# Performance work log

Measured on AMD Instinct MI355X. Metric: run time of the kernel, lower is better.

Reference implementation:

```python
import jax, jax.numpy as jnp
import numpy as np
import math

HIDDEN = 1024
N_HEAD = 16
D_K = HIDDEN // N_HEAD

def setup_inputs() -> dict:
    key = jax.random.key(0)
    ks = jax.random.split(key, 6)
    B, T = 2, 2048
    x = jax.random.normal(ks[0], (B, T, HIDDEN), dtype=jnp.float32)
    mask = jax.random.randint(ks[1], (B, 1, 1, T), 0, 2, dtype=jnp.int32)
    s = 1.0 / math.sqrt(HIDDEN)
    W_qkv = jax.random.normal(ks[2], (HIDDEN, 3 * HIDDEN), dtype=jnp.float32) * s
    b_qkv = jnp.zeros((3 * HIDDEN,), dtype=jnp.float32)
    W_out = jax.random.normal(ks[3], (HIDDEN, HIDDEN), dtype=jnp.float32) * s
    b_out = jnp.zeros((HIDDEN,), dtype=jnp.float32)
    return {"x": x, "mask": mask, "W_qkv": W_qkv, "b_qkv": b_qkv, "W_out": W_out, "b_out": b_out}

def reference(x, mask, W_qkv, b_qkv, W_out, b_out):
    B, T, H = x.shape
    qkv = x @ W_qkv + b_qkv  # [B,T,3H]
    q, k, v = jnp.split(qkv, 3, axis=-1)
    # [B,T,H] -> [B,nh,T,dk]
    def split_heads(t):
        return t.reshape(B, T, N_HEAD, D_K).transpose(0, 2, 1, 3)
    q, k, v = split_heads(q), split_heads(k), split_heads(v)
    scores = jnp.einsum('bhqd,bhkd->bhqk', q, k) / math.sqrt(D_K)
    scores = jnp.where(mask == 0, jnp.float32(-1e9), scores)
    attn = jax.nn.softmax(scores, axis=-1)
    out = jnp.einsum('bhqk,bhkd->bhqd', attn, v)
    out = out.transpose(0, 2, 1, 3).reshape(B, T, H)
    return out @ W_out + b_out
```

## Files before the change

### kernel.cpp

```cpp
#include <hip/hip_runtime.h>
#include <stdint.h>

typedef unsigned short u16;
typedef unsigned int u32;
typedef short bf16x8 __attribute__((ext_vector_type(8)));
typedef float f32x4 __attribute__((ext_vector_type(4)));

#define MFMA16(a, b, c) __builtin_amdgcn_mfma_f32_16x16x32_bf16((a), (b), (c), 0, 0, 0)
#define BAR()                              \
  do {                                     \
    __builtin_amdgcn_sched_barrier(0);     \
    __builtin_amdgcn_s_barrier();          \
    __builtin_amdgcn_sched_barrier(0);     \
  } while (0)

__device__ __forceinline__ u16 f2bf(float f) {
  union { float f; u32 u; } v; v.f = f;
  u32 u = v.u;
  u32 r = (u + 0x7FFFu + ((u >> 16) & 1u)) >> 16;
  return (u16)r;
}
__device__ __forceinline__ float bf2f(u16 h) {
  union { u32 u; float f; } v; v.u = ((u32)h) << 16;
  return v.f;
}
__device__ __forceinline__ u32 cvtpk_bf16(float lo, float hi) {
  u32 r;
  asm("v_cvt_pk_bf16_f32 %0, %1, %2" : "=v"(r) : "v"(lo), "v"(hi));
  return r;
}

__device__ __forceinline__ void gload_lds16(const void* g, void* l) {
  __builtin_amdgcn_global_load_lds(
      (const __attribute__((address_space(1))) unsigned int*)g,
      (__attribute__((address_space(3))) unsigned int*)l,
      16, 0, 0);
}

__global__ __launch_bounds__(256) void transpose_f32_bf16(
    const float* __restrict__ src, u16* __restrict__ dst, int R, int C) {
  __shared__ u16 t[32][33];
  const int bx = blockIdx.x * 32, by = blockIdx.y * 32;
  const int tx = threadIdx.x & 31, ty = threadIdx.x >> 5;
#pragma unroll
  for (int i = 0; i < 32; i += 8)
    t[ty + i][tx] = f2bf(src[(size_t)(by + ty + i) * C + bx + tx]);
  __syncthreads();
#pragma unroll
  for (int i = 0; i < 32; i += 8)
    dst[(size_t)(bx + ty + i) * R + by + tx] = t[tx][ty + i];
}

__global__ __launch_bounds__(512) void mask_compact(
    const int* __restrict__ mask, int* __restrict__ idx, int* __restrict__ cnt) {
  const int b = blockIdx.x;
  const int tid = threadIdx.x;
  const int lane = tid & 63, wave = tid >> 6;
  __shared__ int wtot[8];
  int m[4], c = 0;
#pragma unroll
  for (int j = 0; j < 4; ++j) {
    m[j] = (mask[b * 2048 + tid * 4 + j] != 0);
    c += m[j];
  }
  int pfx = c;
#pragma unroll
  for (int sh = 1; sh < 64; sh <<= 1) {
    int v = __shfl_up(pfx, sh);
    if (lane >= sh) pfx += v;
  }
  if (lane == 63) wtot[wave] = pfx;
  int epfx = pfx - c;
  __syncthreads();
  int wbase = 0, total = 0;
#pragma unroll
  for (int w = 0; w < 8; ++w) {
    int v = wtot[w];
    if (w < wave) wbase += v;
    total += v;
  }
  int pos = b * 2048 + wbase + epfx;
#pragma unroll
  for (int j = 0; j < 4; ++j)
    if (m[j]) idx[pos++] = tid * 4 + j;
  for (int i = total + tid; i < 2048; i += 512) idx[b * 2048 + i] = 0;
  if (tid == 0) cnt[b] = total;
}

__global__ __launch_bounds__(256) void gemm_a32_bf16(
    const float* __restrict__ A, const u16* __restrict__ Bt,
    const float* __restrict__ bias, u16* __restrict__ Cout,
    int M, int N, int K) {
  __shared__ __align__(16) u16 As[2][128 * 64];
  __shared__ __align__(16) u16 Bs[2][128 * 64];
  const int tid = threadIdx.x;
  const int lane = tid & 63;
  const int wave = tid >> 6;
  const int nwg = gridDim.x;
  const int id = blockIdx.x;
  const int sw = (id & 7) * (nwg >> 3) + (id >> 3);
  const int nx = N >> 7;
  const int m0 = (sw / nx) * 128;
  const int n0 = (sw % nx) * 128;
  const int wm = (wave >> 1) * 64;
  const int wn = (wave & 1) * 64;

  f32x4 acc[4][4] = {};
  const char* Bbase = (const char*)Bt;
  float4 fa[4], fb[4];

#define A32_ISSUE_B(ktile, buf)                                                \
  _Pragma("unroll") for (int i = 0; i < 4; ++i) {                              \
    int flat = wave * 1024 + lane * 16 + i * 4096;                             \
    int row = flat >> 7;                                                       \
    int cb = flat & 127;                                                       \
    int scb = cb ^ ((row & 7) << 4);                                           \
    gload_lds16(Bbase + ((size_t)(n0 + row) * K + (ktile)) * 2 + scb,          \
                (char*)&Bs[buf][0] + flat);                                    \
  }

#define A32_LOAD_A(ktile)                                                      \
  _Pragma("unroll") for (int i = 0; i < 4; ++i) {                              \
    int flat = wave * 1024 + lane * 16 + i * 4096;                             \
    int row = flat >> 7;                                                       \
    int cb = flat & 127;                                                       \
    const float* ax = A + (size_t)(m0 + row) * K + (ktile) + (cb >> 1);        \
    fa[i] = *(const float4*)ax;                                                \
    fb[i] = *(const float4*)(ax + 4);                                          \
  }

#define A32_CVT(buf)                                                           \
  _Pragma("unroll") for (int i = 0; i < 4; ++i) {                              \
    int flat = wave * 1024 + lane * 16 + i * 4096;                             \
    int row = flat >> 7;                                                       \
    int cb = flat & 127;                                                       \
    union { u32 w[4]; bf16x8 v; } o;                                           \
    o.w[0] = cvtpk_bf16(fa[i].x, fa[i].y);                                     \
    o.w[1] = cvtpk_bf16(fa[i].z, fa[i].w);                                     \
    o.w[2] = cvtpk_bf16(fb[i].x, fb[i].y);                                     \
    o.w[3] = cvtpk_bf16(fb[i].z, fb[i].w);                                     \
    *(bf16x8*)((char*)&As[buf][0] + row * 128 + (cb ^ ((row & 7) << 4))) = o.v; \
  }

  A32_ISSUE_B(0, 0);
  A32_LOAD_A(0);
  A32_CVT(0);
  asm volatile("s_waitcnt lgkmcnt(0)" ::: "memory");
  BAR();

  const int nsteps = K >> 6;
  for (int t = 0; t < nsteps; ++t) {
    if (t < nsteps - 1) {
      A32_ISSUE_B((t << 6) + 64, (t & 1) ^ 1);
      A32_LOAD_A((t << 6) + 64);
    }
    __builtin_amdgcn_sched_barrier(0);
#pragma unroll
    for (int ks = 0; ks < 2; ++ks) {
      const int col = (lane >> 4) * 8 + ks * 32;
      bf16x8 af[4], bfr[4];
#pragma unroll
      for (int mt = 0; mt < 4; ++mt) {
        int row = wm + mt * 16 + (lane & 15);
        af[mt] = *(const bf16x8*)((const char*)&As[t & 1][0] + row * 128 +
                                  ((col * 2) ^ ((row & 7) << 4)));
      }
#pragma unroll
      for (int nt = 0; nt < 4; ++nt) {
        int row = wn + nt * 16 + (lane & 15);
        bfr[nt] = *(const bf16x8*)((const char*)&Bs[t & 1][0] + row * 128 +
                                   ((col * 2) ^ ((row & 7) << 4)));
      }
#pragma unroll
      for (int mt = 0; mt < 4; ++mt)
#pragma unroll
        for (int nt = 0; nt < 4; ++nt)
          acc[mt][nt] = MFMA16(af[mt], bfr[nt], acc[mt][nt]);
    }
    __builtin_amdgcn_sched_barrier(0);
    if (t < nsteps - 1) {
      A32_CVT((t & 1) ^ 1);
      asm volatile("s_waitcnt lgkmcnt(0)" ::: "memory");
      BAR();
    }
  }
#undef A32_ISSUE_B
#undef A32_LOAD_A
#undef A32_CVT

  float bv[4];
#pragma unroll
  for (int nt = 0; nt < 4; ++nt)
    bv[nt] = bias[n0 + wn + nt * 16 + (lane & 15)];
#pragma unroll
  for (int mt = 0; mt < 4; ++mt)
#pragma unroll
    for (int nt = 0; nt < 4; ++nt)
#pragma unroll
      for (int r = 0; r < 4; ++r) {
        int m = m0 + wm + mt * 16 + (lane >> 4) * 4 + r;
        int n = n0 + wn + nt * 16 + (lane & 15);
        Cout[(size_t)m * N + n] = f2bf(acc[mt][nt][r] + bv[nt]);
      }
}

template <bool OUT_BF16>
__global__ __launch_bounds__(256) void gemm_bf16(
    const u16* __restrict__ A, const u16* __restrict__ Bt,
    const float* __restrict__ bias, void* __restrict__ Cout,
    int M, int N, int K) {
  __shared__ __align__(16) u16 As[2][128 * 64];
  __shared__ __align__(16) u16 Bs[2][128 * 64];
  const int tid = threadIdx.x;
  const int lane = tid & 63;
  const int wave = tid >> 6;
  const int nwg = gridDim.x;
  const int id = blockIdx.x;
  const int sw = (id & 7) * (nwg >> 3) + (id >> 3);
  const int nx = N >> 7;
  const int m0 = (sw / nx) * 128;
  const int n0 = (sw % nx) * 128;
  const int wm = (wave >> 1) * 64;
  const int wn = (wave & 1) * 64;

  f32x4 acc[4][4] = {};

  const char* Abase = (const char*)A;
  const char* Bbase = (const char*)Bt;

#define STAGE_AB(ktile, buf)                                                   \
  _Pragma("unroll") for (int i = 0; i < 4; ++i) {                              \
    int flat = wave * 1024 + lane * 16 + i * 4096;                             \
    int row = flat >> 7;                                                       \
    int cb = flat & 127;                                                       \
    int scb = cb ^ ((row & 7) << 4);                                           \
    gload_lds16(Abase + ((size_t)(m0 + row) * K + (ktile)) * 2 + scb,          \
                (char*)&As[buf][0] + flat);                                    \
    gload_lds16(Bbase + ((size_t)(n0 + row) * K + (ktile)) * 2 + scb,          \
                (char*)&Bs[buf][0] + flat);                                    \
  }

  STAGE_AB(0, 0);

  const int nsteps = K >> 6;
  for (int t = 0; t < nsteps; ++t) {
    asm volatile("s_waitcnt vmcnt(0)" ::: "memory");
    BAR();
    if (t < nsteps - 1) STAGE_AB((t << 6) + 64, (t & 1) ^ 1);
#pragma unroll
    for (int ks = 0; ks < 2; ++ks) {
      const int col = (lane >> 4) * 8 + ks * 32;
      bf16x8 af[4], bfr[4];
#pragma unroll
      for (int mt = 0; mt < 4; ++mt) {
        int row = wm + mt * 16 + (lane & 15);
        af[mt] = *(const bf16x8*)((const char*)&As[t & 1][0] + row * 128 +
                                  ((col * 2) ^ ((row & 7) << 4)));
      }
#pragma unroll
      for (int nt = 0; nt < 4; ++nt) {
        int row = wn + nt * 16 + (lane & 15);
        bfr[nt] = *(const bf16x8*)((const char*)&Bs[t & 1][0] + row * 128 +
                                   ((col * 2) ^ ((row & 7) << 4)));
      }
#pragma unroll
      for (int mt = 0; mt < 4; ++mt)
#pragma unroll
        for (int nt = 0; nt < 4; ++nt)
          acc[mt][nt] = MFMA16(af[mt], bfr[nt], acc[mt][nt]);
    }
  }
#undef STAGE_AB

  float bv[4];
#pragma unroll
  for (int nt = 0; nt < 4; ++nt)
    bv[nt] = bias[n0 + wn + nt * 16 + (lane & 15)];
#pragma unroll
  for (int mt = 0; mt < 4; ++mt)
#pragma unroll
    for (int nt = 0; nt < 4; ++nt)
#pragma unroll
      for (int r = 0; r < 4; ++r) {
        int m = m0 + wm + mt * 16 + (lane >> 4) * 4 + r;
        int n = n0 + wn + nt * 16 + (lane & 15);
        float v = acc[mt][nt][r] + bv[nt];
        if (OUT_BF16)
          ((u16*)Cout)[(size_t)m * N + n] = f2bf(v);
        else
          ((float*)Cout)[(size_t)m * N + n] = v;
      }
}

#define T_SEQ 2048
#define ROWQKV 3072
#define SCL 0.180336880f

template <bool SPLIT>
__global__ __launch_bounds__(512) void attn_fwd(
    const u16* __restrict__ qkv, const int* __restrict__ idx,
    const int* __restrict__ cnt, u16* __restrict__ outp,
    float* __restrict__ Ml) {
  __shared__ __align__(16) u16 Ks[2][2][64 * 64];
  __shared__ __align__(16) u16 Vt[2][2][64 * 64];
  __shared__ __align__(16) u32 lut[256 * 4];

  const int tid = threadIdx.x;
  const int lane = tid & 63;
  const int wave = tid >> 6;
  const int r15 = lane & 15;
  const int g = lane >> 4;
  const int id = blockIdx.x;
  const int hz = ((id >> 6) << 3) | (id & 7);
  const int qb = (id >> 3) & 7;
  const int h = SPLIT ? (hz >> 2) : (hz >> 1);
  const int z = SPLIT ? (hz & 3) : (hz & 1);
  const int split = SPLIT ? (z >> 1) : 0;
  const int b = SPLIT ? (z & 1) : z;
  const int q0 = qb * 256 + wave * 32;
  const size_t rowb = (size_t)b * T_SEQ;
  const int* idxb = idx + b * 2048;
  const int count = cnt[b];
  const int ntot = (count + 127) >> 7;
  const int nth = (ntot + 1) >> 1;
  const int t0 = (SPLIT && split) ? nth : 0;
  const int nt2 = SPLIT ? (split ? ntot - nth : nth) : ntot;

  for (int i = tid; i < 256; i += 512) {
    union { u32 w[4]; bf16x8 v; } e;
#pragma unroll
    for (int j = 0; j < 4; ++j)
      e.w[j] = (((i >> (2 * j)) & 1) ? 0x3F80u : 0u) |
               (((i >> (2 * j + 1)) & 1) ? 0x3F800000u : 0u);
    *(bf16x8*)((char*)lut + i * 16) = e.v;
  }

  bf16x8 aq[2][2];
#pragma unroll
  for (int mt = 0; mt < 2; ++mt)
#pragma unroll
    for (int ks = 0; ks < 2; ++ks) {
      bf16x8 t = *(const bf16x8*)(qkv +
          (rowb + q0 + mt * 16 + r15) * ROWQKV + h * 64 + g * 8 + ks * 32);
#pragma unroll
      for (int j = 0; j < 8; ++j) t[j] = (short)f2bf(bf2f((u16)t[j]) * SCL);
      aq[mt][ks] = t;
    }

  f32x4 accO[2][4] = {};
  f32x4 ssum[2] = {};
  bf16x8 vr0, vr1;

#define ISSUE_K2(ct, buf)                                                      \
  {                                                                            \
    int L = wave * 1024 + lane * 16;                                           \
    int row = L >> 7;                                                          \
    int cb = L & 127;                                                          \
    int scb = cb ^ ((row & 7) << 4);                                           \
    int prow = ((row >> 4) & 1) * 32 + ((row >> 2) & 3) * 8 +                  \
               (row >> 5) * 4 + (row & 3);                                     \
    int gk0 = idxb[(ct) * 128 + prow];                                         \
    int gk1 = idxb[(ct) * 128 + 64 + prow];                                    \
    gload_lds16((const char*)qkv +                                             \
                    ((rowb + gk0) * ROWQKV + 1024 + h * 64) * 2 + scb,         \
                (char*)&Ks[buf][0][0] + wave * 1024);                          \
    gload_lds16((const char*)qkv +                                             \
                    ((rowb + gk1) * ROWQKV + 1024 + h * 64) * 2 + scb,         \
                (char*)&Ks[buf][1][0] + wave * 1024);                          \
  }

#define LOAD_V2(ct)                                                            \
  {                                                                            \
    int key = tid >> 3;                                                        \
    int gv0 = idxb[(ct) * 128 + key];                                          \
    int gv1 = idxb[(ct) * 128 + 64 + key];                                     \
    vr0 = *(const bf16x8*)(qkv + (rowb + gv0) * ROWQKV + 2048 + h * 64 +       \
                           (tid & 7) * 8);                                     \
    vr1 = *(const bf16x8*)(qkv + (rowb + gv1) * ROWQKV + 2048 + h * 64 +       \
                           (tid & 7) * 8);                                     \
  }

#define WRITE_V2(buf, ct)                                                      \
  {                                                                            \
    int key = tid >> 3;                                                        \
    if ((ct) * 128 + key >= count) {                                           \
      bf16x8 zz = {};                                                          \
      vr0 = zz;                                                                \
    }                                                                          \
    if ((ct) * 128 + 64 + key >= count) {                                      \
      bf16x8 zz = {};                                                          \
      vr1 = zz;                                                                \
    }                                                                          \
    _Pragma("unroll") for (int j = 0; j < 8; ++j) {                            \
      int row = (tid & 7) * 8 + j;                                             \
      int sv = ((row ^ (row >> 3)) & 7) << 4;                                  \
      *(u16*)((char*)&Vt[buf][0][0] + row * 128 + ((key * 2) ^ sv)) =          \
          (u16)vr0[j];                                                         \
      *(u16*)((char*)&Vt[buf][1][0] + row * 128 + ((key * 2) ^ sv)) =          \
          (u16)vr1[j];                                                         \
    }                                                                          \
  }

#define COMPUTE_HALF(H, ct)                                                    \
  {                                                                            \
    f32x4 s[2][4] = {};                                                        \
    _Pragma("unroll") for (int ks = 0; ks < 2; ++ks) {                         \
      bf16x8 bk[4];                                                            \
      _Pragma("unroll") for (int nt = 0; nt < 4; ++nt) {                       \
        int row = nt * 16 + r15;                                               \
        int cb = (g * 8 + ks * 32) * 2;                                        \
        bk[nt] = *(const bf16x8*)((const char*)&Ks[cur][H][0] + row * 128 +    \
                                  (cb ^ ((row & 7) << 4)));                    \
      }                                                                        \
      _Pragma("unroll") for (int mt = 0; mt < 2; ++mt)                         \
        _Pragma("unroll") for (int nt = 0; nt < 4; ++nt)                       \
          s[mt][nt] = MFMA16(bk[nt], aq[mt][ks], s[mt][nt]);                   \
    }                                                                          \
    u32 pk[2][4][2];                                                           \
    _Pragma("unroll") for (int mt = 0; mt < 2; ++mt)                           \
      _Pragma("unroll") for (int nt = 0; nt < 4; ++nt) {                       \
        float e0 = exp2f(s[mt][nt][0]);                                        \
        float e1 = exp2f(s[mt][nt][1]);                                        \
        float e2 = exp2f(s[mt][nt][2]);                                        \
        float e3 = exp2f(s[mt][nt][3]);                                        \
        pk[mt][nt][0] = cvtpk_bf16(e0, e1);                                    \
        pk[mt][nt][1] = cvtpk_bf16(e2, e3);                                    \
      }                                                                        \
    __builtin_amdgcn_s_setprio(1);                                             \
    _Pragma("unroll") for (int ks = 0; ks < 2; ++ks) {                         \
      const int col = g * 8 + ks * 32;                                         \
      bf16x8 bv[4];                                                            \
      _Pragma("unroll") for (int nt = 0; nt < 4; ++nt) {                       \
        int row = nt * 16 + r15;                                               \
        int sv = ((row ^ (row >> 3)) & 7) << 4;                                \
        bv[nt] = *(const bf16x8*)((const char*)&Vt[cur][H][0] + row * 128 +    \
                                  ((col * 2) ^ sv));                           \
      }                                                                        \
      int rbase = count - ((ct) * 128 + (H) * 64 + ks * 32 + g * 8);           \
      int rr = rbase < 0 ? 0 : (rbase > 8 ? 8 : rbase);                        \
      u32 lb = (1u << rr) - 1u;                                                \
      bf16x8 mf = *(const bf16x8*)((const char*)lut + lb * 16);                \
      _Pragma("unroll") for (int mt = 0; mt < 2; ++mt) {                       \
        union { u32 w[4]; bf16x8 v; } ap;                                      \
        ap.w[0] = pk[mt][ks][0];                                               \
        ap.w[1] = pk[mt][ks][1];                                               \
        ap.w[2] = pk[mt][2 + ks][0];                                           \
        ap.w[3] = pk[mt][2 + ks][1];                                           \
        _Pragma("unroll") for (int nt = 0; nt < 4; ++nt)                       \
          accO[mt][nt] = MFMA16(ap.v, bv[nt], accO[mt][nt]);                   \
        ssum[mt] = MFMA16(ap.v, mf, ssum[mt]);                                 \
      }                                                                        \
    }                                                                          \
    __builtin_amdgcn_s_setprio(0);                                             \
  }

  if (nt2 > 0) {
    ISSUE_K2(t0, 0);
    LOAD_V2(t0);
    __syncthreads();
    WRITE_V2(0, t0);
    asm volatile("s_waitcnt lgkmcnt(0)" ::: "memory");
    BAR();

    int cur = 0;
    for (int t = 0; t < nt2; ++t) {
      const int ct = t0 + t;
      if (t < nt2 - 1) {
        ISSUE_K2(ct + 1, cur ^ 1);
        LOAD_V2(ct + 1);
      }

      COMPUTE_HALF(0, ct);
      COMPUTE_HALF(1, ct);

      if (t < nt2 - 1) {
        asm volatile("s_waitcnt vmcnt(0)" ::: "memory");
        WRITE_V2(cur ^ 1, ct + 1);
        asm volatile("s_waitcnt lgkmcnt(0)" ::: "memory");
        BAR();
        cur ^= 1;
      }
    }
  }

  if (SPLIT) {
    u16* po = outp + (size_t)split * T_SEQ * 2 * 1024;
#pragma unroll
    for (int mt = 0; mt < 2; ++mt) {
#pragma unroll
      for (int r = 0; r < 4; ++r) {
        int q = q0 + mt * 16 + g * 4 + r;
#pragma unroll
        for (int nt = 0; nt < 4; ++nt)
          po[(rowb + q) * 1024 + h * 64 + nt * 16 + r15] = f2bf(accO[mt][nt][r]);
      }
      if (r15 == 0) {
        int idxm = ((split * 2 + b) * 16 + h) * T_SEQ + q0 + mt * 16 + g * 4;
        *(f32x4*)(Ml + idxm) = ssum[mt];
      }
    }
  } else {
#pragma unroll
    for (int mt = 0; mt < 2; ++mt)
#pragma unroll
      for (int r = 0; r < 4; ++r) {
        float inv = 1.f / ssum[mt][r];
        int q = q0 + mt * 16 + g * 4 + r;
#pragma unroll
        for (int nt = 0; nt < 4; ++nt)
          outp[(rowb + q) * 1024 + h * 64 + nt * 16 + r15] =
              f2bf(accO[mt][nt][r] * inv);
      }
  }
#undef ISSUE_K2
#undef LOAD_V2
#undef WRITE_V2
#undef COMPUTE_HALF
}

__global__ __launch_bounds__(256) void attn_combine(
    const u16* __restrict__ part, const float* __restrict__ Ml,
    u16* __restrict__ att) {
  int idx = blockIdx.x * 256 + threadIdx.x;
  int row = idx >> 7;
  int c8 = idx & 127;
  int col = c8 * 8;
  int h = c8 >> 3;
  int b = row >> 11, q = row & 2047;
  float l0 = Ml[(b * 16 + h) * T_SEQ + q];
  float l1 = Ml[((2 + b) * 16 + h) * T_SEQ + q];
  float inv = 1.f / (l0 + l1);
  bf16x8 o0 = *(const bf16x8*)(part + (size_t)row * 1024 + col);
  bf16x8 o1 = *(const bf16x8*)(part + (size_t)T_SEQ * 2 * 1024 +
                               (size_t)row * 1024 + col);
  bf16x8 o;
#pragma unroll
  for (int j = 0; j < 8; ++j)
    o[j] = (short)f2bf((bf2f((u16)o0[j]) + bf2f((u16)o1[j])) * inv);
  *(bf16x8*)(att + (size_t)row * 1024 + col) = o;
}

extern "C" void kernel_launch(void* const* d_in, const int* in_sizes, int n_in,
                              void* d_out, int out_size, void* d_ws, size_t ws_size,
                              hipStream_t stream) {
  const float* x = (const float*)d_in[0];
  const int* mask = (const int*)d_in[1];
  const float* Wqkv = (const float*)d_in[2];
  const float* bqkv = (const float*)d_in[3];
  const float* Wout = (const float*)d_in[4];
  const float* bout = (const float*)d_in[5];
  float* out = (float*)d_out;

  const int B = 2, T = 2048, H = 1024, M = B * T;

  u16* qkv = (u16*)d_ws;
  u16* att = qkv + (size_t)M * 3 * H;
  u16* WtQ = att + (size_t)M * H;
  u16* WtO = WtQ + (size_t)3 * H * H;
  u16* part = WtO + (size_t)H * H;
  float* Ml = (float*)(part + (size_t)2 * M * H);
  int* idxb = (int*)(Ml + (size_t)2 * 131072);
  int* cntb = idxb + B * T;

  const size_t need = ((size_t)M * 3 * H + (size_t)M * H + (size_t)3 * H * H +
                       (size_t)H * H + (size_t)2 * M * H) * 2 +
                      (size_t)2 * 131072 * 4 + (size_t)(B * T + 8) * 4;
  const bool split = ws_size >= need;

  transpose_f32_bf16<<<dim3(3 * H / 32, H / 32), 256, 0, stream>>>(Wqkv, WtQ, H, 3 * H);
  transpose_f32_bf16<<<dim3(H / 32, H / 32), 256, 0, stream>>>(Wout, WtO, H, H);
  mask_compact<<<B, 512, 0, stream>>>(mask, idxb, cntb);
  gemm_a32_bf16<<<(3 * H / 128) * (M / 128), 256, 0, stream>>>(x, WtQ, bqkv, qkv, M, 3 * H, H);
  if (split) {
    attn_fwd<true><<<512, 512, 0, stream>>>(qkv, idxb, cntb, part, Ml);
    attn_combine<<<(M * H / 8 + 255) / 256, 256, 0, stream>>>(part, Ml, att);
  } else {
    attn_fwd<false><<<256, 512, 0, stream>>>(qkv, idxb, cntb, att, Ml);
  }
  gemm_bf16<false><<<(H / 128) * (M / 128), 256, 0, stream>>>(att, WtO, bout, out, M, H, H);
}
```

Baseline: 133.5 us.

## Deepen QKV GEMM prefetch to two k-tiles ahead with triple-buffered B

Adds a third LDS buffer for B and a second set of fp32 A staging registers so global loads run two k-steps ahead of compute instead of one. The loop is unrolled by two to alternate the register sets. This is meant to hide more global-memory latency behind the MFMA work. The cost is extra LDS and more registers, which may lower occupancy. The loop also assumes nsteps is even.

```diff
diff --git a/kernel.cpp b/kernel.cpp
--- a/kernel.cpp
+++ b/kernel.cpp
@@ -92,7 +92,7 @@
     const float* __restrict__ bias, u16* __restrict__ Cout,
     int M, int N, int K) {
   __shared__ __align__(16) u16 As[2][128 * 64];
-  __shared__ __align__(16) u16 Bs[2][128 * 64];
+  __shared__ __align__(16) u16 Bs[3][128 * 64];
   const int tid = threadIdx.x;
   const int lane = tid & 63;
   const int wave = tid >> 6;
@@ -107,7 +107,7 @@
 
   f32x4 acc[4][4] = {};
   const char* Bbase = (const char*)Bt;
-  float4 fa[4], fb[4];
+  float4 fa0[4], fb0[4], fa1[4], fb1[4];
 
 #define A32_ISSUE_B(ktile, buf)                                                \
   _Pragma("unroll") for (int i = 0; i < 4; ++i) {                              \
@@ -119,71 +119,80 @@
                 (char*)&Bs[buf][0] + flat);                                    \
   }
 
-#define A32_LOAD_A(ktile)                                                      \
+#define A32_LOAD_A(ktile, FA, FB)                                              \
   _Pragma("unroll") for (int i = 0; i < 4; ++i) {                              \
     int flat = wave * 1024 + lane * 16 + i * 4096;                             \
     int row = flat >> 7;                                                       \
     int cb = flat & 127;                                                       \
     const float* ax = A + (size_t)(m0 + row) * K + (ktile) + (cb >> 1);        \
-    fa[i] = *(const float4*)ax;                                                \
-    fb[i] = *(const float4*)(ax + 4);                                          \
-  }
-
-#define A32_CVT(buf)                                                           \
+    FA[i] = *(const float4*)ax;                                                \
+    FB[i] = *(const float4*)(ax + 4);                                          \
+  }
+
+#define A32_CVT(FA, FB, buf)                                                   \
   _Pragma("unroll") for (int i = 0; i < 4; ++i) {                              \
     int flat = wave * 1024 + lane * 16 + i * 4096;                             \
     int row = flat >> 7;                                                       \
     int cb = flat & 127;                                                       \
     union { u32 w[4]; bf16x8 v; } o;                                           \
-    o.w[0] = cvtpk_bf16(fa[i].x, fa[i].y);                                     \
-    o.w[1] = cvtpk_bf16(fa[i].z, fa[i].w);                                     \
-    o.w[2] = cvtpk_bf16(fb[i].x, fb[i].y);                                     \
-    o.w[3] = cvtpk_bf16(fb[i].z, fb[i].w);                                     \
+    o.w[0] = cvtpk_bf16(FA[i].x, FA[i].y);                                     \
+    o.w[1] = cvtpk_bf16(FA[i].z, FA[i].w);                                     \
+    o.w[2] = cvtpk_bf16(FB[i].x, FB[i].y);                                     \
+    o.w[3] = cvtpk_bf16(FB[i].z, FB[i].w);                                     \
     *(bf16x8*)((char*)&As[buf][0] + row * 128 + (cb ^ ((row & 7) << 4))) = o.v; \
   }
 
+  const int nsteps = K >> 6;
+
   A32_ISSUE_B(0, 0);
-  A32_LOAD_A(0);
-  A32_CVT(0);
+  A32_LOAD_A(0, fa0, fb0);
+  A32_ISSUE_B(64, 1);
+  A32_LOAD_A(64, fa1, fb1);
+  A32_CVT(fa0, fb0, 0);
   asm volatile("s_waitcnt lgkmcnt(0)" ::: "memory");
   BAR();
 
-  const int nsteps = K >> 6;
-  for (int t = 0; t < nsteps; ++t) {
-    if (t < nsteps - 1) {
-      A32_ISSUE_B((t << 6) + 64, (t & 1) ^ 1);
-      A32_LOAD_A((t << 6) + 64);
-    }
-    __builtin_amdgcn_sched_barrier(0);
-#pragma unroll
-    for (int ks = 0; ks < 2; ++ks) {
-      const int col = (lane >> 4) * 8 + ks * 32;
-      bf16x8 af[4], bfr[4];
-#pragma unroll
-      for (int mt = 0; mt < 4; ++mt) {
-        int row = wm + mt * 16 + (lane & 15);
-        af[mt] = *(const bf16x8*)((const char*)&As[t & 1][0] + row * 128 +
-                                  ((col * 2) ^ ((row & 7) << 4)));
-      }
-#pragma unroll
-      for (int nt = 0; nt < 4; ++nt) {
-        int row = wn + nt * 16 + (lane & 15);
-        bfr[nt] = *(const bf16x8*)((const char*)&Bs[t & 1][0] + row * 128 +
-                                   ((col * 2) ^ ((row & 7) << 4)));
-      }
-#pragma unroll
-      for (int mt = 0; mt < 4; ++mt)
-#pragma unroll
-        for (int nt = 0; nt < 4; ++nt)
-          acc[mt][nt] = MFMA16(af[mt], bfr[nt], acc[mt][nt]);
-    }
-    __builtin_amdgcn_sched_barrier(0);
-    if (t < nsteps - 1) {
-      A32_CVT((t & 1) ^ 1);
-      asm volatile("s_waitcnt lgkmcnt(0)" ::: "memory");
-      BAR();
-    }
-  }
+#define QSTEP(T, FA_L, FB_L, FA_C, FB_C)                                       \
+  {                                                                            \
+    if ((T) + 2 < nsteps) {                                                    \
+      A32_ISSUE_B(((T) + 2) << 6, ((T) + 2) % 3);                              \
+      A32_LOAD_A(((T) + 2) << 6, FA_L, FB_L);                                  \
+    }                                                                          \
+    __builtin_amdgcn_sched_barrier(0);                                         \
+    {                                                                          \
+      const u16* BsT = &Bs[(T) % 3][0];                                        \
+      const u16* AsT = &As[(T) & 1][0];                                        \
+      _Pragma("unroll") for (int ks = 0; ks < 2; ++ks) {                       \
+        const int col = (lane >> 4) * 8 + ks * 32;                             \
+        bf16x8 af[4], bfr[4];                                                  \
+        _Pragma("unroll") for (int mt = 0; mt < 4; ++mt) {                     \
+          int row = wm + mt * 16 + (lane & 15);                                \
+          af[mt] = *(const bf16x8*)((const char*)AsT + row * 128 +             \
+                                    ((col * 2) ^ ((row & 7) << 4)));           \
+        }                                                                      \
+        _Pragma("unroll") for (int nt = 0; nt < 4; ++nt) {                     \
+          int row = wn + nt * 16 + (lane & 15);                                \
+          bfr[nt] = *(const bf16x8*)((const char*)BsT + row * 128 +            \
+                                     ((col * 2) ^ ((row & 7) << 4)));          \
+        }                                                                      \
+        _Pragma("unroll") for (int mt = 0; mt < 4; ++mt)                       \
+          _Pragma("unroll") for (int nt = 0; nt < 4; ++nt)                     \
+            acc[mt][nt] = MFMA16(af[mt], bfr[nt], acc[mt][nt]);                \
+      }                                                                        \
+    }                                                                          \
+    __builtin_amdgcn_sched_barrier(0);                                         \
+    if ((T) + 1 < nsteps) {                                                    \
+      A32_CVT(FA_C, FB_C, ((T) + 1) & 1);                                      \
+      asm volatile("s_waitcnt lgkmcnt(0)" ::: "memory");                       \
+      BAR();                                                                   \
+    }                                                                          \
+  }
+
+  for (int tt = 0; tt < nsteps; tt += 2) {
+    QSTEP(tt, fa0, fb0, fa1, fb1);
+    QSTEP(tt + 1, fa1, fb1, fa0, fb0);
+  }
+#undef QSTEP
 #undef A32_ISSUE_B
 #undef A32_LOAD_A
 #undef A32_CVT
```

Measured after the change: 151.5 us. 1.13x slower.
